# Kernel optimization log

Measured on AMD Instinct MI355X. Metric: run time of the kernel, lower is better.

The kernel has to match this reference:

```python
import jax, jax.numpy as jnp
import numpy as np

B, S, D_IN, D_H = 8, 2048, 1024, 1024

def setup_inputs() -> dict:
    key = jax.random.key(0)
    ks = jax.random.split(key, 7)
    scale = 1.0 / np.sqrt(D_IN)
    return {
        "x": jax.random.normal(ks[0], (B, S, D_IN), dtype=jnp.float32),
        "Wq": jax.random.uniform(ks[1], (D_IN, D_H), jnp.float32, -scale, scale),
        "bq": jax.random.uniform(ks[2], (D_H,), jnp.float32, -scale, scale),
        "Wk": jax.random.uniform(ks[3], (D_IN, D_H), jnp.float32, -scale, scale),
        "bk": jax.random.uniform(ks[4], (D_H,), jnp.float32, -scale, scale),
        "Wv": jax.random.uniform(ks[5], (D_IN, D_H), jnp.float32, -scale, scale),
        "bv": jax.random.uniform(ks[6], (D_H,), jnp.float32, -scale, scale),
    }

def reference(x, Wq, bq, Wk, bk, Wv, bv):
    # q, k, v: [B, S, D_H]
    q = jnp.einsum('bsd,dh->bsh', x, Wq) + bq
    k = jnp.einsum('bsd,dh->bsh', x, Wk) + bk
    v = jnp.einsum('bsd,dh->bsh', x, Wv) + bv
    inv_sqrt_d = 1.0 / jnp.sqrt(jnp.asarray(D_H, x.dtype))
    scores = jnp.einsum('bqh,bkh->bqk', q, k) * inv_sqrt_d  # [B, S, S]
    attn = jax.nn.softmax(scores, axis=-1)
    return jnp.einsum('bqk,bkh->bqh', attn, v)
```

## Files before the change

### kernel.cpp

```cpp
#include <hip/hip_runtime.h>

typedef __attribute__((ext_vector_type(8))) short short8;
typedef __attribute__((ext_vector_type(4))) short short4v;
typedef __attribute__((ext_vector_type(4))) float f32x4;
typedef unsigned int u32;

#define AS1 __attribute__((address_space(1)))
#define AS3 __attribute__((address_space(3)))

__device__ __forceinline__ short f2bf(float x){
  union { float f; u32 u; } v; v.f = x;
  u32 r = (v.u + 0x7FFFu + ((v.u >> 16) & 1u)) >> 16;
  return (short)r;
}
__device__ __forceinline__ float bf2f(short s){
  union { u32 u; float f; } v; v.u = ((u32)(unsigned short)s) << 16;
  return v.f;
}
__device__ __forceinline__ void gload16(const void* src, void* dst){
  __builtin_amdgcn_global_load_lds((const AS1 u32*)src, (AS3 u32*)dst, 16, 0, 0);
}

__global__ __launch_bounds__(256) void cvt_x_kernel(const float* __restrict__ x, short* __restrict__ xb){
  int i = blockIdx.x * 256 + threadIdx.x;
  if (i >= 2097152) return;
  const float4* xf = (const float4*)x;
  float4 a = xf[2*i], b = xf[2*i+1];
  short8 o;
  o[0]=f2bf(a.x); o[1]=f2bf(a.y); o[2]=f2bf(a.z); o[3]=f2bf(a.w);
  o[4]=f2bf(b.x); o[5]=f2bf(b.y); o[6]=f2bf(b.z); o[7]=f2bf(b.w);
  ((short8*)xb)[i] = o;
}

__global__ __launch_bounds__(256) void cvt_w_kernel(const float* __restrict__ Wq, const float* __restrict__ Wk,
                                                    const float* __restrict__ Wv, short* __restrict__ Wt){
  __shared__ float tile[32][33];
  const float* W = blockIdx.z == 0 ? Wq : (blockIdx.z == 1 ? Wk : Wv);
  short* out = Wt + (size_t)blockIdx.z * 1024 * 1024;
  int n0 = blockIdx.x * 32, k0 = blockIdx.y * 32;
  int tx = threadIdx.x, ty = threadIdx.y;
  #pragma unroll
  for (int i=0;i<4;i++) tile[ty + 8*i][tx] = W[(size_t)(k0 + ty + 8*i) * 1024 + n0 + tx];
  __syncthreads();
  #pragma unroll
  for (int i=0;i<4;i++) out[(size_t)(n0 + ty + 8*i) * 1024 + k0 + tx] = f2bf(tile[tx][ty + 8*i]);
}

template<int EPI>
__global__ __launch_bounds__(512, 2)
void gemm256(const short* __restrict__ A, int lda, long abst,
             const short* __restrict__ B, int ldb, long bbst,
             void* __restrict__ Cv, long cbst,
             const float* __restrict__ bias0, const float* __restrict__ bias1,
             int M, int N, int K, float scale)
{
  __shared__ alignas(16) short As[32768];
  __shared__ alignas(16) short Bs[32768];

  const u32 nx = gridDim.x, ny = gridDim.y;
  const u32 id  = blockIdx.x + nx * (blockIdx.y + ny * blockIdx.z);
  const u32 nwg = nx * ny * gridDim.z;
  const u32 id2 = (id & 7) * (nwg >> 3) + (id >> 3);
  const u32 bx = id2 % nx;
  const u32 rem = id2 / nx;
  const u32 by = rem % ny;
  const u32 z  = rem / ny;

  A += (size_t)z * abst;
  B += (size_t)z * bbst;
  const int m0 = bx * 256, n0 = by * 256;
  const int tid = threadIdx.x;
  const int w = tid >> 6, l = tid & 63;
  const int wm = w >> 2, wn = w & 3;
  const int lr = l & 15, l4 = l >> 4;
  const u32 sw = (u32)(l & 7) << 4;
  const u32 koff0 = ((u32)l4 << 4) ^ sw;
  const u32 koff1 = koff0 ^ 64u;
  const size_t lda2 = (size_t)lda * 2, ldb2 = (size_t)ldb * 2;

  f32x4 acc[8][4];
  #pragma unroll
  for (int i=0;i<8;i++)
    #pragma unroll
    for (int j=0;j<4;j++) acc[i][j] = (f32x4){0.f,0.f,0.f,0.f};

  const int r0 = tid >> 3;
  const int c8 = (tid & 7) ^ (r0 & 7);
  const char* Asrc = (const char*)A + (size_t)(m0 + r0) * lda2 + c8 * 16;
  const char* Bsrc = (const char*)B + (size_t)(n0 + r0) * ldb2 + c8 * 16;
  char* AD = (char*)As + (w * 64) * 16;
  char* BD = (char*)Bs + (w * 64) * 16;

  const int NT = K >> 6;

  auto stage = [&](int T, int p){
    const char* aS = Asrc + (size_t)T * 128;
    const char* bS = Bsrc + (size_t)T * 128;
    char* aD = AD + p * 32768;
    char* bD = BD + p * 32768;
    #pragma unroll
    for (int i = 0; i < 4; i++){
      gload16(aS + (size_t)(i*64) * lda2, aD + i * 8192);
      gload16(bS + (size_t)(i*64) * ldb2, bD + i * 8192);
    }
  };

  stage(0, 0);
  stage(1, 1);

  for (int T = 0; T < NT; T++){
    const int p = T & 1;
    if (T < NT - 1) asm volatile("s_waitcnt vmcnt(8)" ::: "memory");
    else            asm volatile("s_waitcnt vmcnt(0)" ::: "memory");
    __builtin_amdgcn_s_barrier();

    const char* aR = (const char*)As + p * 32768 + (wm * 128 + lr) * 128;
    const char* bR = (const char*)Bs + p * 32768 + (wn * 64 + lr) * 128;
    short8 fa[2][8], fb[2][4];
    #pragma unroll
    for (int j = 0; j < 4; j++){
      fb[0][j] = *(const short8*)(bR + j * 2048 + koff0);
      fb[1][j] = *(const short8*)(bR + j * 2048 + koff1);
    }
    #pragma unroll
    for (int i = 0; i < 8; i++){
      fa[0][i] = *(const short8*)(aR + i * 2048 + koff0);
      fa[1][i] = *(const short8*)(aR + i * 2048 + koff1);
    }

    __builtin_amdgcn_s_setprio(1);
    #pragma unroll
    for (int kh = 0; kh < 2; kh++)
      #pragma unroll
      for (int i = 0; i < 8; i++)
        #pragma unroll
        for (int j = 0; j < 4; j++)
          acc[i][j] = __builtin_amdgcn_mfma_f32_16x16x32_bf16(fa[kh][i], fb[kh][j], acc[i][j], 0, 0, 0);
    __builtin_amdgcn_s_setprio(0);

    asm volatile("s_waitcnt lgkmcnt(0)" ::: "memory");
    __builtin_amdgcn_s_barrier();
    if (T + 2 < NT) stage(T + 2, p);
  }

  const int mwb = m0 + wm*128 + l4*4;
  const int nwb = n0 + wn*64 + lr;

  if constexpr (EPI == 0){
    const float* bias = z ? bias1 : bias0;
    short* C = (short*)Cv + (size_t)z * cbst;
    float bvv[4];
    #pragma unroll
    for (int j=0;j<4;j++) bvv[j] = bias[nwb + j*16];
    #pragma unroll
    for (int i=0;i<8;i++){
      int m = mwb + i*16;
      #pragma unroll
      for (int j=0;j<4;j++){
        int n = nwb + j*16;
        #pragma unroll
        for (int r=0;r<4;r++)
          C[(size_t)(m+r)*N + n] = f2bf(acc[i][j][r] + bvv[j]);
      }
    }
  } else if constexpr (EPI == 1){
    short* C = (short*)Cv;
    float bvv[4];
    #pragma unroll
    for (int j=0;j<4;j++) bvv[j] = bias0[nwb + j*16];
    #pragma unroll
    for (int i=0;i<8;i++){
      int m = mwb + i*16;
      int bidx = m >> 11, ml = m & 2047;
      #pragma unroll
      for (int j=0;j<4;j++){
        int n = nwb + j*16;
        short4v pk;
        #pragma unroll
        for (int r=0;r<4;r++) pk[r] = f2bf(acc[i][j][r] + bvv[j]);
        *(short4v*)&C[((size_t)(bidx*1024 + n)) * 2048 + ml] = pk;
      }
    }
  } else if constexpr (EPI == 2){
    short* C = (short*)Cv + (size_t)z * cbst;
    #pragma unroll
    for (int i=0;i<8;i++){
      int m = mwb + i*16;
      #pragma unroll
      for (int j=0;j<4;j++){
        int n = nwb + j*16;
        #pragma unroll
        for (int r=0;r<4;r++)
          C[(size_t)(m+r)*N + n] = f2bf(acc[i][j][r] * scale);
      }
    }
  } else {
    float* C = (float*)Cv + (size_t)z * cbst;
    #pragma unroll
    for (int i=0;i<8;i++){
      int m = mwb + i*16;
      #pragma unroll
      for (int j=0;j<4;j++){
        int n = nwb + j*16;
        #pragma unroll
        for (int r=0;r<4;r++)
          C[(size_t)(m+r)*N + n] = acc[i][j][r];
      }
    }
  }
}

__global__ __launch_bounds__(256) void softmax_kernel(short* __restrict__ S){
  const int row = blockIdx.x;
  short* p = S + (size_t)row * 2048;
  const int t = threadIdx.x, w = t >> 6, l = t & 63;
  short8 v = *(short8*)&p[t*8];
  float f[8];
  #pragma unroll
  for (int i=0;i<8;i++) f[i] = bf2f(v[i]);
  float mx = f[0];
  #pragma unroll
  for (int i=1;i<8;i++) mx = fmaxf(mx, f[i]);
  #pragma unroll
  for (int off=32; off>=1; off>>=1) mx = fmaxf(mx, __shfl_xor(mx, off));
  __shared__ float rmax[4], rsum[4];
  if (l == 0) rmax[w] = mx;
  __syncthreads();
  mx = fmaxf(fmaxf(rmax[0], rmax[1]), fmaxf(rmax[2], rmax[3]));
  float e[8], s = 0.f;
  #pragma unroll
  for (int i=0;i<8;i++){ e[i] = __expf(f[i] - mx); s += e[i]; }
  #pragma unroll
  for (int off=32; off>=1; off>>=1) s += __shfl_xor(s, off);
  if (l == 0) rsum[w] = s;
  __syncthreads();
  s = rsum[0] + rsum[1] + rsum[2] + rsum[3];
  float inv = 1.0f / s;
  short8 o;
  #pragma unroll
  for (int i=0;i<8;i++) o[i] = f2bf(e[i] * inv);
  *(short8*)&p[t*8] = o;
}

extern "C" void kernel_launch(void* const* d_in, const int* in_sizes, int n_in,
                              void* d_out, int out_size, void* d_ws, size_t ws_size,
                              hipStream_t stream){
  (void)in_sizes; (void)n_in; (void)out_size;
  const float* x  = (const float*)d_in[0];
  const float* Wq = (const float*)d_in[1];
  const float* bq = (const float*)d_in[2];
  const float* Wk = (const float*)d_in[3];
  const float* bk = (const float*)d_in[4];
  const float* Wv = (const float*)d_in[5];
  const float* bv = (const float*)d_in[6];
  float* out = (float*)d_out;
  char* ws = (char*)d_ws;

  short* qb  = (short*)(ws + 0);
  short* kb  = (short*)(ws + 33554432);
  short* vt  = (short*)(ws + 67108864);
  short* xb  = (short*)(ws + 100663296);
  short* Wt  = (short*)(ws + 134217728);
  short* Sg  = xb;
  const bool big = ws_size >= (size_t)167772160;

  cvt_x_kernel<<<8192, 256, 0, stream>>>(x, xb);
  cvt_w_kernel<<<dim3(32,32,3), dim3(32,8), 0, stream>>>(Wq, Wk, Wv, Wt);

  gemm256<0><<<dim3(64,4,2), 512, 0, stream>>>(xb, 1024, 0L, Wt, 1024, 1048576L,
                                               qb, 16777216L, bq, bk, 16384, 1024, 1024, 1.f);
  gemm256<1><<<dim3(64,4,1), 512, 0, stream>>>(xb, 1024, 0L, Wt + 2*1048576, 1024, 0L,
                                               vt, 0L, bv, nullptr, 16384, 1024, 1024, 1.f);

  if (big){
    gemm256<2><<<dim3(8,8,8), 512, 0, stream>>>(qb, 1024, 2097152L, kb, 1024, 2097152L,
                                                Sg, 4194304L, nullptr, nullptr,
                                                2048, 2048, 1024, 0.03125f);
    softmax_kernel<<<16384, 256, 0, stream>>>(Sg);
    gemm256<3><<<dim3(8,4,8), 512, 0, stream>>>(Sg, 2048, 4194304L, vt, 2048, 2097152L,
                                                out, 2097152L, nullptr, nullptr,
                                                2048, 1024, 2048, 1.f);
  } else {
    for (int g = 0; g < 2; g++){
      const size_t boff = (size_t)g * 4 * 2097152;
      gemm256<2><<<dim3(8,8,4), 512, 0, stream>>>(qb + boff, 1024, 2097152L,
                                                  kb + boff, 1024, 2097152L,
                                                  Sg, 4194304L, nullptr, nullptr,
                                                  2048, 2048, 1024, 0.03125f);
      softmax_kernel<<<8192, 256, 0, stream>>>(Sg);
      gemm256<3><<<dim3(8,4,4), 512, 0, stream>>>(Sg, 2048, 4194304L,
                                                  vt + boff, 2048, 2097152L,
                                                  out + boff, 2097152L, nullptr, nullptr,
                                                  2048, 1024, 2048, 1.f);
    }
  }
}
```

Baseline: 409.5 us.

## Split GEMM main loop into four MFMA phases interleaved with half-tile loads

Rewrites the 256x256 GEMM inner loop as a four-phase, ping-pong style schedule. LDS tiles are split into halves, so each phase reads a subset of A/B fragments, issues the next tile's global-to-LDS loads for one half, and runs 16 MFMAs under barriers with raised priority. The aim is to overlap global loads and LDS reads with MFMA work and cut register pressure from holding all fragments. The change also drops the large-workspace path and always runs attention in two batch groups, which adds launches but reduces the score buffer footprint.

```diff
diff --git a/kernel.cpp b/kernel.cpp
--- a/kernel.cpp
+++ b/kernel.cpp
@@ -20,6 +20,7 @@
 __device__ __forceinline__ void gload16(const void* src, void* dst){
   __builtin_amdgcn_global_load_lds((const AS1 u32*)src, (AS3 u32*)dst, 16, 0, 0);
 }
+#define MFMA_(a,b,c) c = __builtin_amdgcn_mfma_f32_16x16x32_bf16(a, b, c, 0, 0, 0)
 
 __global__ __launch_bounds__(256) void cvt_x_kernel(const float* __restrict__ x, short* __restrict__ xb){
   int i = blockIdx.x * 256 + threadIdx.x;
@@ -73,8 +74,7 @@
   const int w = tid >> 6, l = tid & 63;
   const int wm = w >> 2, wn = w & 3;
   const int lr = l & 15, l4 = l >> 4;
-  const u32 sw = (u32)(l & 7) << 4;
-  const u32 koff0 = ((u32)l4 << 4) ^ sw;
+  const u32 koff0 = ((u32)l4 << 4) ^ ((u32)(l & 7) << 4);
   const u32 koff1 = koff0 ^ 64u;
   const size_t lda2 = (size_t)lda * 2, ldb2 = (size_t)ldb * 2;
 
@@ -84,63 +84,104 @@
     #pragma unroll
     for (int j=0;j<4;j++) acc[i][j] = (f32x4){0.f,0.f,0.f,0.f};
 
-  const int r0 = tid >> 3;
-  const int c8 = (tid & 7) ^ (r0 & 7);
-  const char* Asrc = (const char*)A + (size_t)(m0 + r0) * lda2 + c8 * 16;
-  const char* Bsrc = (const char*)B + (size_t)(n0 + r0) * ldb2 + c8 * 16;
-  char* AD = (char*)As + (w * 64) * 16;
-  char* BD = (char*)Bs + (w * 64) * 16;
+  const int c8 = (tid & 7) ^ ((tid >> 3) & 7);
+  const char* ASrcB = (const char*)A + (size_t)(m0 + (tid >> 3)) * lda2 + c8 * 16;
+  const char* BSrcB = (const char*)B + (size_t)(n0 + (tid >> 3)) * ldb2 + c8 * 16;
+  char* dstA0 = (char*)As + tid * 16;
+  char* dstB0 = (char*)Bs + tid * 16;
 
   const int NT = K >> 6;
 
-  auto stage = [&](int T, int p){
-    const char* aS = Asrc + (size_t)T * 128;
-    const char* bS = Bsrc + (size_t)T * 128;
-    char* aD = AD + p * 32768;
-    char* bD = BD + p * 32768;
-    #pragma unroll
-    for (int i = 0; i < 4; i++){
-      gload16(aS + (size_t)(i*64) * lda2, aD + i * 8192);
-      gload16(bS + (size_t)(i*64) * ldb2, bD + i * 8192);
-    }
+  auto stA = [&](int tile, int h){
+    const char* s = ASrcB + (size_t)(h * 128) * lda2 + (size_t)tile * 128;
+    char* dd = dstA0 + ((tile & 1) * 2 + h) * 16384;
+    gload16(s,             dd);
+    gload16(s + 64 * lda2, dd + 8192);
   };
-
-  stage(0, 0);
-  stage(1, 1);
+  auto stB = [&](int tile, int h){
+    const char* s = BSrcB + (size_t)(h * 128) * ldb2 + (size_t)tile * 128;
+    char* dd = dstB0 + ((tile & 1) * 2 + h) * 16384;
+    gload16(s,             dd);
+    gload16(s + 64 * ldb2, dd + 8192);
+  };
+
+  stA(0,0); stA(0,1); stB(0,0); stB(0,1);
+  if (NT > 1){ stA(1,0); asm volatile("s_waitcnt vmcnt(2)" ::: "memory"); }
+  else       {           asm volatile("s_waitcnt vmcnt(0)" ::: "memory"); }
+  __builtin_amdgcn_s_barrier();
 
   for (int T = 0; T < NT; T++){
-    const int p = T & 1;
-    if (T < NT - 1) asm volatile("s_waitcnt vmcnt(8)" ::: "memory");
-    else            asm volatile("s_waitcnt vmcnt(0)" ::: "memory");
-    __builtin_amdgcn_s_barrier();
-
-    const char* aR = (const char*)As + p * 32768 + (wm * 128 + lr) * 128;
-    const char* bR = (const char*)Bs + p * 32768 + (wn * 64 + lr) * 128;
-    short8 fa[2][8], fb[2][4];
-    #pragma unroll
-    for (int j = 0; j < 4; j++){
-      fb[0][j] = *(const short8*)(bR + j * 2048 + koff0);
-      fb[1][j] = *(const short8*)(bR + j * 2048 + koff1);
-    }
-    #pragma unroll
-    for (int i = 0; i < 8; i++){
-      fa[0][i] = *(const short8*)(aR + i * 2048 + koff0);
-      fa[1][i] = *(const short8*)(aR + i * 2048 + koff1);
-    }
-
+    const int d = T & 1;
+    const char* aB = (const char*)As + (d*2 + wm) * 16384 + lr * 128;
+    const char* bB = (const char*)Bs + (d*2 + (wn >> 1)) * 16384 + ((wn & 1) * 64 + lr) * 128;
+    short8 fa0[4], fa1[4], fb0[4], fb1[4];
+
+    #pragma unroll
+    for (int ii=0; ii<4; ii++){
+      fa0[ii] = *(const short8*)(aB + ii*2048 + koff0);
+      fa1[ii] = *(const short8*)(aB + ii*2048 + koff1);
+    }
+    fb0[0] = *(const short8*)(bB + koff0);        fb1[0] = *(const short8*)(bB + koff1);
+    fb0[1] = *(const short8*)(bB + 2048 + koff0); fb1[1] = *(const short8*)(bB + 2048 + koff1);
+    if (T + 1 < NT) stA(T+1, 1);
+    asm volatile("s_waitcnt lgkmcnt(8)" ::: "memory");
+    __builtin_amdgcn_s_barrier();
+    asm volatile("s_waitcnt lgkmcnt(0)" ::: "memory");
+    __builtin_amdgcn_sched_barrier(0);
     __builtin_amdgcn_s_setprio(1);
     #pragma unroll
-    for (int kh = 0; kh < 2; kh++)
-      #pragma unroll
-      for (int i = 0; i < 8; i++)
-        #pragma unroll
-        for (int j = 0; j < 4; j++)
-          acc[i][j] = __builtin_amdgcn_mfma_f32_16x16x32_bf16(fa[kh][i], fb[kh][j], acc[i][j], 0, 0, 0);
+    for (int ii=0; ii<4; ii++){
+      MFMA_(fa0[ii], fb0[0], acc[ii][0]);  MFMA_(fa1[ii], fb1[0], acc[ii][0]);
+      MFMA_(fa0[ii], fb0[1], acc[ii][1]);  MFMA_(fa1[ii], fb1[1], acc[ii][1]);
+    }
     __builtin_amdgcn_s_setprio(0);
-
+    __builtin_amdgcn_s_barrier();
+
+    fb0[2] = *(const short8*)(bB + 2*2048 + koff0); fb1[2] = *(const short8*)(bB + 2*2048 + koff1);
+    fb0[3] = *(const short8*)(bB + 3*2048 + koff0); fb1[3] = *(const short8*)(bB + 3*2048 + koff1);
+    if (T + 1 < NT) stB(T+1, 0);
+    __builtin_amdgcn_s_barrier();
     asm volatile("s_waitcnt lgkmcnt(0)" ::: "memory");
-    __builtin_amdgcn_s_barrier();
-    if (T + 2 < NT) stage(T + 2, p);
+    __builtin_amdgcn_sched_barrier(0);
+    __builtin_amdgcn_s_setprio(1);
+    #pragma unroll
+    for (int ii=0; ii<4; ii++){
+      MFMA_(fa0[ii], fb0[2], acc[ii][2]);  MFMA_(fa1[ii], fb1[2], acc[ii][2]);
+      MFMA_(fa0[ii], fb0[3], acc[ii][3]);  MFMA_(fa1[ii], fb1[3], acc[ii][3]);
+    }
+    __builtin_amdgcn_s_setprio(0);
+    __builtin_amdgcn_s_barrier();
+
+    #pragma unroll
+    for (int ii=0; ii<4; ii++){
+      fa0[ii] = *(const short8*)(aB + 8192 + ii*2048 + koff0);
+      fa1[ii] = *(const short8*)(aB + 8192 + ii*2048 + koff1);
+    }
+    if (T + 1 < NT) stB(T+1, 1);
+    __builtin_amdgcn_s_barrier();
+    asm volatile("s_waitcnt lgkmcnt(0)" ::: "memory");
+    __builtin_amdgcn_sched_barrier(0);
+    __builtin_amdgcn_s_setprio(1);
+    #pragma unroll
+    for (int ii=0; ii<4; ii++){
+      MFMA_(fa0[ii], fb0[2], acc[4+ii][2]);  MFMA_(fa1[ii], fb1[2], acc[4+ii][2]);
+      MFMA_(fa0[ii], fb0[3], acc[4+ii][3]);  MFMA_(fa1[ii], fb1[3], acc[4+ii][3]);
+    }
+    __builtin_amdgcn_s_setprio(0);
+    __builtin_amdgcn_s_barrier();
+
+    if (T + 2 < NT){ stA(T+2, 0); asm volatile("s_waitcnt vmcnt(2)" ::: "memory"); }
+    else           {             asm volatile("s_waitcnt vmcnt(0)" ::: "memory"); }
+    __builtin_amdgcn_s_barrier();
+    __builtin_amdgcn_sched_barrier(0);
+    __builtin_amdgcn_s_setprio(1);
+    #pragma unroll
+    for (int ii=0; ii<4; ii++){
+      MFMA_(fa0[ii], fb0[0], acc[4+ii][0]);  MFMA_(fa1[ii], fb1[0], acc[4+ii][0]);
+      MFMA_(fa0[ii], fb0[1], acc[4+ii][1]);  MFMA_(fa1[ii], fb1[1], acc[4+ii][1]);
+    }
+    __builtin_amdgcn_s_setprio(0);
+    __builtin_amdgcn_s_barrier();
   }
 
   const int mwb = m0 + wm*128 + l4*4;
@@ -245,7 +286,7 @@
 extern "C" void kernel_launch(void* const* d_in, const int* in_sizes, int n_in,
                               void* d_out, int out_size, void* d_ws, size_t ws_size,
                               hipStream_t stream){
-  (void)in_sizes; (void)n_in; (void)out_size;
+  (void)in_sizes; (void)n_in; (void)out_size; (void)ws_size;
   const float* x  = (const float*)d_in[0];
   const float* Wq = (const float*)d_in[1];
   const float* bq = (const float*)d_in[2];
@@ -262,7 +303,6 @@
   short* xb  = (short*)(ws + 100663296);
   short* Wt  = (short*)(ws + 134217728);
   short* Sg  = xb;
-  const bool big = ws_size >= (size_t)167772160;
 
   cvt_x_kernel<<<8192, 256, 0, stream>>>(x, xb);
   cvt_w_kernel<<<dim3(32,32,3), dim3(32,8), 0, stream>>>(Wq, Wk, Wv, Wt);
@@ -272,26 +312,16 @@
   gemm256<1><<<dim3(64,4,1), 512, 0, stream>>>(xb, 1024, 0L, Wt + 2*1048576, 1024, 0L,
                                                vt, 0L, bv, nullptr, 16384, 1024, 1024, 1.f);
 
-  if (big){
-    gemm256<2><<<dim3(8,8,8), 512, 0, stream>>>(qb, 1024, 2097152L, kb, 1024, 2097152L,
+  for (int g = 0; g < 2; g++){
+    const size_t boff = (size_t)g * 4 * 2097152;
+    gemm256<2><<<dim3(8,8,4), 512, 0, stream>>>(qb + boff, 1024, 2097152L,
+                                                kb + boff, 1024, 2097152L,
                                                 Sg, 4194304L, nullptr, nullptr,
                                                 2048, 2048, 1024, 0.03125f);
-    softmax_kernel<<<16384, 256, 0, stream>>>(Sg);
-    gemm256<3><<<dim3(8,4,8), 512, 0, stream>>>(Sg, 2048, 4194304L, vt, 2048, 2097152L,
-                                                out, 2097152L, nullptr, nullptr,
+    softmax_kernel<<<8192, 256, 0, stream>>>(Sg);
+    gemm256<3><<<dim3(8,4,4), 512, 0, stream>>>(Sg, 2048, 4194304L,
+                                                vt + boff, 2048, 2097152L,
+                                                out + boff, 2097152L, nullptr, nullptr,
                                                 2048, 1024, 2048, 1.f);
-  } else {
-    for (int g = 0; g < 2; g++){
-      const size_t boff = (size_t)g * 4 * 2097152;
-      gemm256<2><<<dim3(8,8,4), 512, 0, stream>>>(qb + boff, 1024, 2097152L,
-                                                  kb + boff, 1024, 2097152L,
-                                                  Sg, 4194304L, nullptr, nullptr,
-                                                  2048, 2048, 1024, 0.03125f);
-      softmax_kernel<<<8192, 256, 0, stream>>>(Sg);
-      gemm256<3><<<dim3(8,4,4), 512, 0, stream>>>(Sg, 2048, 4194304L,
-                                                  vt + boff, 2048, 2097152L,
-                                                  out + boff, 2097152L, nullptr, nullptr,
-                                                  2048, 1024, 2048, 1.f);
-    }
   }
 }
```

Measured after the change: 468.2 us. +14.3%, slower.
